# Optimization experiments

Measured on AMD Instinct MI355X. Metric: run time of the kernel, lower is better.

The kernel has to match this reference:

```python
import jax, jax.numpy as jnp
import numpy as np
from jax import lax

T, B, E = 128, 32, 4096
H = 512            # hidden per direction
K = 20             # tagset size
START, STOP = 18, 19
NEG = -10000.0


def setup_inputs() -> dict:
    key = jax.random.key(0)
    ks = jax.random.split(key, 12)
    s = 0.02
    x = jax.random.normal(ks[0], (T, B, E), dtype=jnp.float32)
    tags = jax.random.randint(ks[1], (B, T), 0, 18)  # gold tags, exclude START/STOP
    W_e2n = jax.random.normal(ks[2], (E, E), dtype=jnp.float32) * s
    b_e2n = jnp.zeros((E,), jnp.float32)
    # LSTM params, torch gate order (i, f, g, o); biases b_ih + b_hh fused
    W_ih_f = jax.random.normal(ks[3], (4 * H, E), dtype=jnp.float32) * s
    W_hh_f = jax.random.normal(ks[4], (4 * H, H), dtype=jnp.float32) * s
    b_f = jnp.zeros((4 * H,), jnp.float32)
    W_ih_b = jax.random.normal(ks[5], (4 * H, E), dtype=jnp.float32) * s
    W_hh_b = jax.random.normal(ks[6], (4 * H, H), dtype=jnp.float32) * s
    b_b = jnp.zeros((4 * H,), jnp.float32)
    W_lin = jax.random.normal(ks[7], (K, 2 * H), dtype=jnp.float32) * s
    b_lin = jnp.zeros((K,), jnp.float32)
    trans = jax.random.normal(ks[8], (K, K), dtype=jnp.float32)
    trans = trans.at[START, :].set(NEG).at[:, STOP].set(NEG)
    return dict(x=x, tags=tags, W_e2n=W_e2n, b_e2n=b_e2n,
                W_ih_f=W_ih_f, W_hh_f=W_hh_f, b_f=b_f,
                W_ih_b=W_ih_b, W_hh_b=W_hh_b, b_b=b_b,
                W_lin=W_lin, b_lin=b_lin, trans=trans)


def _lstm_dir(x, W_ih, W_hh, b, reverse):
    # x: [T, B, E] -> hidden states [T, B, H]
    xg = jnp.einsum('tbe,ge->tbg', x, W_ih) + b  # [T, B, 4H]
    if reverse:
        xg = xg[::-1]
    h0 = jnp.zeros((x.shape[1], W_hh.shape[1]), x.dtype)

    def step(carry, g_x):
        h, c = carry
        g = g_x + h @ W_hh.T
        i, f, gg, o = jnp.split(g, 4, axis=-1)
        i = jax.nn.sigmoid(i); f = jax.nn.sigmoid(f)
        gg = jnp.tanh(gg); o = jax.nn.sigmoid(o)
        c = f * c + i * gg
        h = o * jnp.tanh(c)
        return (h, c), h

    _, hs = lax.scan(step, (h0, h0), xg)
    return hs[::-1] if reverse else hs


def _features(x, W_e2n, b_e2n, W_ih_f, W_hh_f, b_f, W_ih_b, W_hh_b, b_b, W_lin, b_lin):
    # embedding2nn (relearn_embeddings)
    x = jnp.einsum('tbe,fe->tbf', x, W_e2n) + b_e2n
    hf = _lstm_dir(x, W_ih_f, W_hh_f, b_f, reverse=False)
    hb = _lstm_dir(x, W_ih_b, W_hh_b, b_b, reverse=True)
    h = jnp.concatenate([hf, hb], axis=-1)            # [T, B, 2H]
    feats = jnp.einsum('tbh,kh->tbk', h, W_lin) + b_lin  # [T, B, K]
    return jnp.swapaxes(feats, 0, 1)                  # [B, T, K]


def _crf_nll(feats, tags, trans):
    # feats [B, T, K]; trans[i, j] = score(j -> i)
    Bn, Tn, Kn = feats.shape
    alpha0 = jnp.full((Bn, Kn), NEG, feats.dtype).at[:, START].set(0.0)

    def step(alpha, emit):
        # alpha[b, prev] + trans[next, prev], logsumexp over prev, + emission
        scores = alpha[:, None, :] + trans[None, :, :]     # [B, next, prev]
        return jax.nn.logsumexp(scores, axis=2) + emit, None

    alpha, _ = lax.scan(step, alpha0, jnp.swapaxes(feats, 0, 1))
    log_Z = jax.nn.logsumexp(alpha + trans[STOP][None, :], axis=1)  # [B]

    # gold path score
    prev = jnp.concatenate([jnp.full((Bn, 1), START, tags.dtype), tags], axis=1)
    nxt = jnp.concatenate([tags, jnp.full((Bn, 1), STOP, tags.dtype)], axis=1)
    trans_score = trans[nxt, prev].sum(axis=1)
    emit_score = jnp.take_along_axis(feats, tags[:, :, None], axis=2)[..., 0].sum(axis=1)
    return log_Z - (trans_score + emit_score)  # [B]


def reference(x, tags, W_e2n, b_e2n, W_ih_f, W_hh_f, b_f,
              W_ih_b, W_hh_b, b_b, W_lin, b_lin, trans):
    feats = _features(x, W_e2n, b_e2n, W_ih_f, W_hh_f, b_f,
                      W_ih_b, W_hh_b, b_b, W_lin, b_lin)
    return _crf_nll(feats, tags, trans)
```

## Files before the change

### kernel.cpp

```cpp
#include <hip/hip_runtime.h>
#include <hip/hip_cooperative_groups.h>
#include <stdint.h>


#define NEGV (-10000.0f)

namespace cg = cooperative_groups;

typedef __bf16          bf16x8 __attribute__((ext_vector_type(8)));
typedef float           f32x4  __attribute__((ext_vector_type(4)));
typedef unsigned short  u16x8  __attribute__((ext_vector_type(8)));

typedef const __attribute__((address_space(1))) unsigned int* as1p;
typedef __attribute__((address_space(3))) unsigned int* as3p;

__device__ __forceinline__ void lds_cp16(const void* g, void* l) {
  __builtin_amdgcn_global_load_lds((as1p)g, (as3p)l, 16, 0, 0);
}

__device__ __forceinline__ unsigned short f2bf(float f) {
  unsigned int u = __float_as_uint(f);
  u += 0x7fffu + ((u >> 16) & 1u);
  return (unsigned short)(u >> 16);
}
__device__ __forceinline__ float bf2f(unsigned short h) {
  return __uint_as_float(((unsigned int)h) << 16);
}

__global__ __launch_bounds__(256) void cvt_f32_bf16(const float* __restrict__ in,
                                                    unsigned short* __restrict__ out,
                                                    int n4) {
  int stride = gridDim.x * blockDim.x;
  for (int i = blockIdx.x * blockDim.x + threadIdx.x; i < n4; i += stride) {
    float4 f = ((const float4*)in)[i];
    ushort4 o;
    o.x = f2bf(f.x); o.y = f2bf(f.y); o.z = f2bf(f.z); o.w = f2bf(f.w);
    ((ushort4*)out)[i] = o;
  }
}

__global__ __launch_bounds__(256) void gemm_bf16(const unsigned short* __restrict__ A,
                                                 const unsigned short* __restrict__ B,
                                                 unsigned short* __restrict__ C,
                                                 const float* __restrict__ bias0,
                                                 const float* __restrict__ bias1,
                                                 int nsplit, int M, int N, int K) {
  __shared__ unsigned short As[128 * 32];
  __shared__ unsigned short Bs[128 * 32];
  const int tid   = threadIdx.x;
  const int lane  = tid & 63;
  const int wm    = (tid >> 6) >> 1;
  const int wn    = (tid >> 6) & 1;
  const int nb    = N >> 7;
  const int bm    = (int)(blockIdx.x / nb) << 7;
  const int bn    = (int)(blockIdx.x % nb) << 7;
  const int srow  = tid >> 2;
  const int skoff = (tid & 3) * 8;
  const int lrow  = lane & 15;
  const int lk    = (lane >> 4) * 8;

  f32x4 acc[4][4];
#pragma unroll
  for (int i = 0; i < 4; ++i)
#pragma unroll
    for (int j = 0; j < 4; ++j) acc[i][j] = (f32x4){0.f, 0.f, 0.f, 0.f};

  for (int k0 = 0; k0 < K; k0 += 32) {
    lds_cp16(A + (size_t)(bm + srow) * K + k0 + skoff,      &As[tid * 8]);
    lds_cp16(A + (size_t)(bm + 64 + srow) * K + k0 + skoff, &As[2048 + tid * 8]);
    lds_cp16(B + (size_t)(bn + srow) * K + k0 + skoff,      &Bs[tid * 8]);
    lds_cp16(B + (size_t)(bn + 64 + srow) * K + k0 + skoff, &Bs[2048 + tid * 8]);
    __syncthreads();
    bf16x8 af[4], bfr[4];
#pragma unroll
    for (int mi = 0; mi < 4; ++mi)
      af[mi] = *(const bf16x8*)&As[(wm * 64 + mi * 16 + lrow) * 32 + lk];
#pragma unroll
    for (int ni = 0; ni < 4; ++ni)
      bfr[ni] = *(const bf16x8*)&Bs[(wn * 64 + ni * 16 + lrow) * 32 + lk];
#pragma unroll
    for (int mi = 0; mi < 4; ++mi)
#pragma unroll
      for (int ni = 0; ni < 4; ++ni)
        acc[mi][ni] = __builtin_amdgcn_mfma_f32_16x16x32_bf16(af[mi], bfr[ni], acc[mi][ni], 0, 0, 0);
    __syncthreads();
  }

#pragma unroll
  for (int mi = 0; mi < 4; ++mi) {
#pragma unroll
    for (int ni = 0; ni < 4; ++ni) {
      const int col = bn + wn * 64 + ni * 16 + lrow;
      const float bv = (col < nsplit) ? bias0[col] : bias1[col - nsplit];
#pragma unroll
      for (int j = 0; j < 4; ++j) {
        const int row = bm + wm * 64 + mi * 16 + (lane >> 4) * 4 + j;
        C[(size_t)row * N + col] = f2bf(acc[mi][ni][j] + bv);
      }
    }
  }
}

__global__ __launch_bounds__(512) void lstm_persist(const unsigned short* __restrict__ Whh,
                                                    const unsigned short* __restrict__ xg,
                                                    unsigned short* __restrict__ hstate,
                                                    unsigned short* __restrict__ hseq) {
  __shared__ unsigned short Wlds[4 * 32 * 520];
  __shared__ float G[4 * 32 * 36];

  cg::grid_group grid = cg::this_grid();

  const int bid  = blockIdx.x;
  const int dir  = bid >> 4;
  const int cgc  = bid & 15;
  const int colbase = cgc * 32;
  const int tid  = threadIdx.x;
  const int lane = tid & 63;
  const int wid  = tid >> 6;
  const int g    = wid & 3;
  const int mh   = wid >> 2;
  const int lrow = lane & 15;
  const int lk4  = lane >> 4;
  const int lk   = lk4 * 8;

  for (int idx = tid; idx < 4 * 32 * 64; idx += 512) {
    const int g2 = idx >> 11;
    const int r  = (idx >> 6) & 31;
    const int c  = idx & 63;
    u16x8 v = *(const u16x8*)&Whh[(size_t)(dir * 2048 + g2 * 512 + colbase + r) * 512 + c * 8];
    *(u16x8*)&Wlds[(g2 * 32 + r) * 520 + c * 8] = v;
  }
  __syncthreads();

  const int b0  = tid >> 5,        col0 = tid & 31;
  const int b1  = (tid + 512) >> 5, col1 = tid & 31;
  float creg0 = 0.f, creg1 = 0.f;

  for (int s = 0; s < 128; ++s) {
    const int t = dir ? (127 - s) : s;

    unsigned short xv0[4], xv1[4];
    {
      const size_t xr0 = (size_t)(t * 32 + b0) * 4096 + dir * 2048 + colbase + col0;
      const size_t xr1 = (size_t)(t * 32 + b1) * 4096 + dir * 2048 + colbase + col1;
#pragma unroll
      for (int g2 = 0; g2 < 4; ++g2) { xv0[g2] = xg[xr0 + g2 * 512]; xv1[g2] = xg[xr1 + g2 * 512]; }
    }

    const unsigned short* hp = hstate + (size_t)((s & 1) * 2 + dir) * 32 * 512;
    u16x8 a[16];
#pragma unroll
    for (int kk = 0; kk < 16; ++kk)
      a[kk] = *(const u16x8*)&hp[(mh * 16 + lrow) * 512 + kk * 32 + lk];

    f32x4 acc[2] = {(f32x4){0.f,0.f,0.f,0.f}, (f32x4){0.f,0.f,0.f,0.f}};
#pragma unroll
    for (int ct = 0; ct < 2; ++ct)
#pragma unroll
      for (int kk = 0; kk < 16; ++kk) {
        u16x8 w = *(const u16x8*)&Wlds[(g * 32 + ct * 16 + lrow) * 520 + kk * 32 + lk];
        acc[ct] = __builtin_amdgcn_mfma_f32_16x16x32_bf16(
            __builtin_bit_cast(bf16x8, a[kk]), __builtin_bit_cast(bf16x8, w), acc[ct], 0, 0, 0);
      }

#pragma unroll
    for (int ct = 0; ct < 2; ++ct)
#pragma unroll
      for (int j = 0; j < 4; ++j)
        G[g * 1152 + (mh * 16 + lk4 * 4 + j) * 36 + ct * 16 + lrow] = acc[ct][j];
    __syncthreads();

    unsigned short* hn = hstate + (size_t)(((s + 1) & 1) * 2 + dir) * 32 * 512;
    {
      float vi = G[0 * 1152 + b0 * 36 + col0] + bf2f(xv0[0]);
      float vf = G[1 * 1152 + b0 * 36 + col0] + bf2f(xv0[1]);
      float vg = G[2 * 1152 + b0 * 36 + col0] + bf2f(xv0[2]);
      float vo = G[3 * 1152 + b0 * 36 + col0] + bf2f(xv0[3]);
      float ig = 1.f / (1.f + expf(-vi));
      float fg = 1.f / (1.f + expf(-vf));
      float gv = tanhf(vg);
      float og = 1.f / (1.f + expf(-vo));
      creg0 = fg * creg0 + ig * gv;
      unsigned short hb = f2bf(og * tanhf(creg0));
      hn[b0 * 512 + colbase + col0] = hb;
      hseq[(size_t)(t * 32 + b0) * 1024 + dir * 512 + colbase + col0] = hb;
    }
    {
      float vi = G[0 * 1152 + b1 * 36 + col1] + bf2f(xv1[0]);
      float vf = G[1 * 1152 + b1 * 36 + col1] + bf2f(xv1[1]);
      float vg = G[2 * 1152 + b1 * 36 + col1] + bf2f(xv1[2]);
      float vo = G[3 * 1152 + b1 * 36 + col1] + bf2f(xv1[3]);
      float ig = 1.f / (1.f + expf(-vi));
      float fg = 1.f / (1.f + expf(-vf));
      float gv = tanhf(vg);
      float og = 1.f / (1.f + expf(-vo));
      creg1 = fg * creg1 + ig * gv;
      unsigned short hb = f2bf(og * tanhf(creg1));
      hn[b1 * 512 + colbase + col1] = hb;
      hseq[(size_t)(t * 32 + b1) * 1024 + dir * 512 + colbase + col1] = hb;
    }

    grid.sync();
  }
}

__global__ __launch_bounds__(256) void feats_gemv(const unsigned short* __restrict__ hseq,
                                                  const float* __restrict__ Wlin,
                                                  const float* __restrict__ blin,
                                                  float* __restrict__ feats) {
  const int lane = threadIdx.x & 63;
  const int wid  = threadIdx.x >> 6;
  const int row  = blockIdx.x * 4 + wid;
  const int t = row >> 5, b = row & 31;
  const unsigned short* hr = hseq + (size_t)row * 1024 + lane * 16;
  float hf[16];
  u16x8 h0 = *(const u16x8*)hr;
  u16x8 h1 = *(const u16x8*)(hr + 8);
#pragma unroll
  for (int i = 0; i < 8; ++i) { hf[i] = bf2f(h0[i]); hf[8 + i] = bf2f(h1[i]); }
  for (int k = 0; k < 20; ++k) {
    const float* wr = Wlin + k * 1024 + lane * 16;
    float p = 0.f;
#pragma unroll
    for (int q = 0; q < 4; ++q) {
      float4 w4 = ((const float4*)wr)[q];
      p += hf[q*4+0]*w4.x + hf[q*4+1]*w4.y + hf[q*4+2]*w4.z + hf[q*4+3]*w4.w;
    }
#pragma unroll
    for (int off = 32; off; off >>= 1) p += __shfl_xor(p, off);
    if (lane == 0) feats[(size_t)b * (128 * 20) + t * 20 + k] = p + blin[k];
  }
}

__global__ __launch_bounds__(64) void crf_nll(const float* __restrict__ feats,
                                              const int* __restrict__ tags,
                                              const float* __restrict__ trans,
                                              float* __restrict__ out) {
  const int b = blockIdx.x;
  const int j = threadIdx.x;
  const bool act = j < 20;
  float tr[20];
#pragma unroll
  for (int p = 0; p < 20; ++p) tr[p] = act ? trans[j * 20 + p] : 0.f;
  float alpha = (j == 18) ? 0.f : NEGV;
  const float* fb = feats + (size_t)b * (128 * 20);
  for (int t = 0; t < 128; ++t) {
    float emit = act ? fb[t * 20 + j] : 0.f;
    float sc[20];
    float m = -1e30f;
#pragma unroll
    for (int p = 0; p < 20; ++p) {
      float ap = __shfl(alpha, p);
      sc[p] = ap + tr[p];
      m = fmaxf(m, sc[p]);
    }
    float sum = 0.f;
#pragma unroll
    for (int p = 0; p < 20; ++p) sum += expf(sc[p] - m);
    alpha = m + logf(sum) + emit;
  }
  float v = act ? (alpha + trans[19 * 20 + j]) : -1e30f;
  float m2 = v;
#pragma unroll
  for (int off = 32; off; off >>= 1) m2 = fmaxf(m2, __shfl_xor(m2, off));
  float s2 = expf(v - m2);
#pragma unroll
  for (int off = 32; off; off >>= 1) s2 += __shfl_xor(s2, off);
  const float logZ = m2 + logf(s2);

  const int* tg = tags + b * 128;
  float ts;
  {
    int prev = (j == 0) ? 18 : tg[j - 1];
    ts = trans[tg[j] * 20 + prev];
    ts += trans[tg[j + 64] * 20 + tg[j + 63]];
    if (j == 0) ts += trans[19 * 20 + tg[127]];
  }
  float es = fb[j * 20 + tg[j]] + fb[(j + 64) * 20 + tg[j + 64]];
  float tot = ts + es;
#pragma unroll
  for (int off = 32; off; off >>= 1) tot += __shfl_xor(tot, off);
  if (j == 0) out[b] = logZ - tot;
}

extern "C" void kernel_launch(void* const* d_in, const int* in_sizes, int n_in,
                              void* d_out, int out_size, void* d_ws, size_t ws_size,
                              hipStream_t stream) {
  const float* x     = (const float*)d_in[0];
  const int*   tags  = (const int*)d_in[1];
  const float* We2n  = (const float*)d_in[2];
  const float* be2n  = (const float*)d_in[3];
  const float* Wihf  = (const float*)d_in[4];
  const float* Whhf  = (const float*)d_in[5];
  const float* bf_   = (const float*)d_in[6];
  const float* Wihb  = (const float*)d_in[7];
  const float* Whhb  = (const float*)d_in[8];
  const float* bb_   = (const float*)d_in[9];
  const float* Wlin  = (const float*)d_in[10];
  const float* blin  = (const float*)d_in[11];
  const float* trans = (const float*)d_in[12];

  char* ws = (char*)d_ws;
  unsigned short* buf0   = (unsigned short*)(ws);
  unsigned short* buf1   = (unsigned short*)(ws + 33554432ULL);
  unsigned short* buf2   = (unsigned short*)(ws + 2ULL * 33554432ULL);
  unsigned short* whhb   = (unsigned short*)(ws + 3ULL * 33554432ULL);
  unsigned short* hseq   = (unsigned short*)(ws + 3ULL * 33554432ULL + 4194304ULL);
  unsigned short* hstate = (unsigned short*)(ws + 3ULL * 33554432ULL + 12582912ULL);
  float*          feats  = (float*)(ws + 3ULL * 33554432ULL + 12845056ULL);

  cvt_f32_bf16<<<2048, 256, 0, stream>>>(x,    buf0, 16777216 / 4);
  cvt_f32_bf16<<<2048, 256, 0, stream>>>(We2n, buf1, 16777216 / 4);
  cvt_f32_bf16<<<512,  256, 0, stream>>>(Whhf, whhb,            1048576 / 4);
  cvt_f32_bf16<<<512,  256, 0, stream>>>(Whhb, whhb + 1048576,  1048576 / 4);
  hipMemsetAsync(hstate, 0, 131072, stream);

  gemm_bf16<<<1024, 256, 0, stream>>>(buf0, buf1, buf2, be2n, be2n, 4096, 4096, 4096, 4096);

  cvt_f32_bf16<<<2048, 256, 0, stream>>>(Wihf, buf1,           8388608 / 4);
  cvt_f32_bf16<<<2048, 256, 0, stream>>>(Wihb, buf1 + 8388608, 8388608 / 4);

  gemm_bf16<<<1024, 256, 0, stream>>>(buf2, buf1, buf0, bf_, bb_, 2048, 4096, 4096, 4096);

  {
    void* args[] = { (void*)&whhb, (void*)&buf0, (void*)&hstate, (void*)&hseq };
    hipLaunchCooperativeKernel((void*)lstm_persist, dim3(32), dim3(512), args, 0, stream);
  }

  feats_gemv<<<1024, 256, 0, stream>>>(hseq, Wlin, blin, feats);

  crf_nll<<<32, 64, 0, stream>>>(feats, tags, trans, (float*)d_out);
}
```

Measured before the change: 2.188 ms.

## Replace grid-wide sync in LSTM recurrence with per-direction flag barriers

Drops the cooperative-groups grid.sync after each timestep. In its place, each of the 16 blocks of a direction sets a per-step flag in global memory and spins until the other 15 blocks of the same direction have set theirs, so the two directions no longer wait on each other. Hidden-state reads and writes now use relaxed agent-scope atomics, and each thread handles two adjacent columns with packed 32-bit loads and stores. The per-step flags are zeroed by a larger memset, and correct visibility depends on the relaxed atomics together with the vmcnt wait.

```diff
diff --git a/kernel.cpp b/kernel.cpp
--- a/kernel.cpp
+++ b/kernel.cpp
@@ -1,11 +1,8 @@
 #include <hip/hip_runtime.h>
-#include <hip/hip_cooperative_groups.h>
 #include <stdint.h>
 
 
 #define NEGV (-10000.0f)
-
-namespace cg = cooperative_groups;
 
 typedef __bf16          bf16x8 __attribute__((ext_vector_type(8)));
 typedef float           f32x4  __attribute__((ext_vector_type(4)));
@@ -104,11 +101,10 @@
 __global__ __launch_bounds__(512) void lstm_persist(const unsigned short* __restrict__ Whh,
                                                     const unsigned short* __restrict__ xg,
                                                     unsigned short* __restrict__ hstate,
-                                                    unsigned short* __restrict__ hseq) {
+                                                    unsigned short* __restrict__ hseq,
+                                                    int* __restrict__ flags) {
   __shared__ unsigned short Wlds[4 * 32 * 520];
   __shared__ float G[4 * 32 * 36];
-
-  cg::grid_group grid = cg::this_grid();
 
   const int bid  = blockIdx.x;
   const int dir  = bid >> 4;
@@ -132,26 +128,33 @@
   }
   __syncthreads();
 
-  const int b0  = tid >> 5,        col0 = tid & 31;
-  const int b1  = (tid + 512) >> 5, col1 = tid & 31;
+  const int bown = tid >> 4;
+  const int c2   = (tid & 15) << 1;
   float creg0 = 0.f, creg1 = 0.f;
+
+  const int arow = (mh * 16 + lrow) * 256 + lk4 * 4;
 
   for (int s = 0; s < 128; ++s) {
     const int t = dir ? (127 - s) : s;
 
-    unsigned short xv0[4], xv1[4];
+    unsigned int xv[4];
     {
-      const size_t xr0 = (size_t)(t * 32 + b0) * 4096 + dir * 2048 + colbase + col0;
-      const size_t xr1 = (size_t)(t * 32 + b1) * 4096 + dir * 2048 + colbase + col1;
-#pragma unroll
-      for (int g2 = 0; g2 < 4; ++g2) { xv0[g2] = xg[xr0 + g2 * 512]; xv1[g2] = xg[xr1 + g2 * 512]; }
-    }
-
-    const unsigned short* hp = hstate + (size_t)((s & 1) * 2 + dir) * 32 * 512;
+      const unsigned short* xr = xg + (size_t)(t * 32 + bown) * 4096 + dir * 2048 + colbase + c2;
+#pragma unroll
+      for (int g2 = 0; g2 < 4; ++g2) xv[g2] = *(const unsigned int*)(xr + g2 * 512);
+    }
+
+    const unsigned int* hp32 = (const unsigned int*)(hstate + (size_t)(((s & 1) * 2 + dir) * 32) * 512);
     u16x8 a[16];
 #pragma unroll
-    for (int kk = 0; kk < 16; ++kk)
-      a[kk] = *(const u16x8*)&hp[(mh * 16 + lrow) * 512 + kk * 32 + lk];
+    for (int kk = 0; kk < 16; ++kk) {
+      uint4 dv;
+      dv.x = __hip_atomic_load(hp32 + arow + kk * 16 + 0, __ATOMIC_RELAXED, __HIP_MEMORY_SCOPE_AGENT);
+      dv.y = __hip_atomic_load(hp32 + arow + kk * 16 + 1, __ATOMIC_RELAXED, __HIP_MEMORY_SCOPE_AGENT);
+      dv.z = __hip_atomic_load(hp32 + arow + kk * 16 + 2, __ATOMIC_RELAXED, __HIP_MEMORY_SCOPE_AGENT);
+      dv.w = __hip_atomic_load(hp32 + arow + kk * 16 + 3, __ATOMIC_RELAXED, __HIP_MEMORY_SCOPE_AGENT);
+      a[kk] = __builtin_bit_cast(u16x8, dv);
+    }
 
     f32x4 acc[2] = {(f32x4){0.f,0.f,0.f,0.f}, (f32x4){0.f,0.f,0.f,0.f}};
 #pragma unroll
@@ -170,37 +173,39 @@
         G[g * 1152 + (mh * 16 + lk4 * 4 + j) * 36 + ct * 16 + lrow] = acc[ct][j];
     __syncthreads();
 
-    unsigned short* hn = hstate + (size_t)(((s + 1) & 1) * 2 + dir) * 32 * 512;
+    unsigned int* hn32 = (unsigned int*)(hstate + (size_t)((((s + 1) & 1) * 2 + dir) * 32) * 512);
     {
-      float vi = G[0 * 1152 + b0 * 36 + col0] + bf2f(xv0[0]);
-      float vf = G[1 * 1152 + b0 * 36 + col0] + bf2f(xv0[1]);
-      float vg = G[2 * 1152 + b0 * 36 + col0] + bf2f(xv0[2]);
-      float vo = G[3 * 1152 + b0 * 36 + col0] + bf2f(xv0[3]);
-      float ig = 1.f / (1.f + expf(-vi));
-      float fg = 1.f / (1.f + expf(-vf));
-      float gv = tanhf(vg);
-      float og = 1.f / (1.f + expf(-vo));
-      creg0 = fg * creg0 + ig * gv;
-      unsigned short hb = f2bf(og * tanhf(creg0));
-      hn[b0 * 512 + colbase + col0] = hb;
-      hseq[(size_t)(t * 32 + b0) * 1024 + dir * 512 + colbase + col0] = hb;
-    }
-    {
-      float vi = G[0 * 1152 + b1 * 36 + col1] + bf2f(xv1[0]);
-      float vf = G[1 * 1152 + b1 * 36 + col1] + bf2f(xv1[1]);
-      float vg = G[2 * 1152 + b1 * 36 + col1] + bf2f(xv1[2]);
-      float vo = G[3 * 1152 + b1 * 36 + col1] + bf2f(xv1[3]);
-      float ig = 1.f / (1.f + expf(-vi));
-      float fg = 1.f / (1.f + expf(-vf));
-      float gv = tanhf(vg);
-      float og = 1.f / (1.f + expf(-vo));
-      creg1 = fg * creg1 + ig * gv;
-      unsigned short hb = f2bf(og * tanhf(creg1));
-      hn[b1 * 512 + colbase + col1] = hb;
-      hseq[(size_t)(t * 32 + b1) * 1024 + dir * 512 + colbase + col1] = hb;
-    }
-
-    grid.sync();
+      float vi0 = G[0 * 1152 + bown * 36 + c2]     + bf2f((unsigned short)(xv[0] & 0xffff));
+      float vi1 = G[0 * 1152 + bown * 36 + c2 + 1] + bf2f((unsigned short)(xv[0] >> 16));
+      float vf0 = G[1 * 1152 + bown * 36 + c2]     + bf2f((unsigned short)(xv[1] & 0xffff));
+      float vf1 = G[1 * 1152 + bown * 36 + c2 + 1] + bf2f((unsigned short)(xv[1] >> 16));
+      float vg0 = G[2 * 1152 + bown * 36 + c2]     + bf2f((unsigned short)(xv[2] & 0xffff));
+      float vg1 = G[2 * 1152 + bown * 36 + c2 + 1] + bf2f((unsigned short)(xv[2] >> 16));
+      float vo0 = G[3 * 1152 + bown * 36 + c2]     + bf2f((unsigned short)(xv[3] & 0xffff));
+      float vo1 = G[3 * 1152 + bown * 36 + c2 + 1] + bf2f((unsigned short)(xv[3] >> 16));
+      float ig0 = 1.f / (1.f + expf(-vi0)), ig1 = 1.f / (1.f + expf(-vi1));
+      float fg0 = 1.f / (1.f + expf(-vf0)), fg1 = 1.f / (1.f + expf(-vf1));
+      float gv0 = tanhf(vg0),               gv1 = tanhf(vg1);
+      float og0 = 1.f / (1.f + expf(-vo0)), og1 = 1.f / (1.f + expf(-vo1));
+      creg0 = fg0 * creg0 + ig0 * gv0;
+      creg1 = fg1 * creg1 + ig1 * gv1;
+      unsigned short h0 = f2bf(og0 * tanhf(creg0));
+      unsigned short h1 = f2bf(og1 * tanhf(creg1));
+      unsigned int hpk = (unsigned int)h0 | ((unsigned int)h1 << 16);
+      __hip_atomic_store(hn32 + bown * 256 + ((colbase + c2) >> 1), hpk,
+                         __ATOMIC_RELAXED, __HIP_MEMORY_SCOPE_AGENT);
+      ((unsigned int*)hseq)[(((size_t)(t * 32 + bown)) * 1024 + dir * 512 + colbase + c2) >> 1] = hpk;
+    }
+
+    asm volatile("s_waitcnt vmcnt(0)" ::: "memory");
+    __syncthreads();
+    const int fbase = (dir * 128 + s) * 16;
+    if (tid == 0)
+      __hip_atomic_store(&flags[fbase + cgc], 1, __ATOMIC_RELAXED, __HIP_MEMORY_SCOPE_AGENT);
+    asm volatile("" ::: "memory");
+    if (tid < 16)
+      while (__hip_atomic_load(&flags[fbase + tid], __ATOMIC_RELAXED, __HIP_MEMORY_SCOPE_AGENT) == 0) {}
+    __syncthreads();
   }
 }
 
@@ -307,13 +312,14 @@
   unsigned short* whhb   = (unsigned short*)(ws + 3ULL * 33554432ULL);
   unsigned short* hseq   = (unsigned short*)(ws + 3ULL * 33554432ULL + 4194304ULL);
   unsigned short* hstate = (unsigned short*)(ws + 3ULL * 33554432ULL + 12582912ULL);
+  int*            flags  = (int*)(ws + 3ULL * 33554432ULL + 12713984ULL);
   float*          feats  = (float*)(ws + 3ULL * 33554432ULL + 12845056ULL);
 
   cvt_f32_bf16<<<2048, 256, 0, stream>>>(x,    buf0, 16777216 / 4);
   cvt_f32_bf16<<<2048, 256, 0, stream>>>(We2n, buf1, 16777216 / 4);
   cvt_f32_bf16<<<512,  256, 0, stream>>>(Whhf, whhb,            1048576 / 4);
   cvt_f32_bf16<<<512,  256, 0, stream>>>(Whhb, whhb + 1048576,  1048576 / 4);
-  hipMemsetAsync(hstate, 0, 131072, stream);
+  hipMemsetAsync(hstate, 0, 147456, stream);
 
   gemm_bf16<<<1024, 256, 0, stream>>>(buf0, buf1, buf2, be2n, be2n, 4096, 4096, 4096, 4096);
 
@@ -323,7 +329,7 @@
   gemm_bf16<<<1024, 256, 0, stream>>>(buf2, buf1, buf0, bf_, bb_, 2048, 4096, 4096, 4096);
 
   {
-    void* args[] = { (void*)&whhb, (void*)&buf0, (void*)&hstate, (void*)&hseq };
+    void* args[] = { (void*)&whhb, (void*)&buf0, (void*)&hstate, (void*)&hseq, (void*)&flags };
     hipLaunchCooperativeKernel((void*)lstm_persist, dim3(32), dim3(512), args, 0, stream);
   }
 
```

Result: slower. 3.015 ms (+37.8%).
